# Kernel tuning notes

Hardware: AMD Instinct MI355X
Metric: run time of the kernel (lower is better)

The kernel has to match this reference:

```python
import jax, jax.numpy as jnp
import numpy as np

B, NS, NW, L, DL, DS, OUT, VOCAB = 32, 8, 32, 196, 1024, 2048, 512, 3266
SCALE = 0.05


def setup_inputs() -> dict:
    key = jax.random.key(0)
    ks = jax.random.split(key, 15)
    r = lambda k, shape: jax.random.normal(k, shape, dtype=jnp.float32)
    return {
        "local_features": r(ks[0], (B, DL, L)),
        "sentenc": r(ks[1], (B, NS, DS)),
        "W_s": r(ks[2], (L, DS)) * SCALE,
        "W_v": r(ks[3], (L, DL)) * SCALE,
        "W_a": r(ks[4], (1, L)) * SCALE,
        "W_ih1": r(ks[5], (4 * OUT, DL)) * SCALE,
        "W_hh1": r(ks[6], (4 * OUT, OUT)) * SCALE,
        "b_ih1": r(ks[7], (4 * OUT,)) * SCALE,
        "b_hh1": r(ks[8], (4 * OUT,)) * SCALE,
        "W_ih2": r(ks[9], (4 * OUT, OUT)) * SCALE,
        "W_hh2": r(ks[10], (4 * OUT, OUT)) * SCALE,
        "b_ih2": r(ks[11], (4 * OUT,)) * SCALE,
        "b_hh2": r(ks[12], (4 * OUT,)) * SCALE,
        "W_f": r(ks[13], (VOCAB, OUT)) * SCALE,
        "b_f": r(ks[14], (VOCAB,)) * SCALE,
    }


def _lstm_cell(x, h, c, W_ih, W_hh, b_ih, b_hh):
    # PyTorch LSTMCell: gates order i, f, g, o
    gates = x @ W_ih.T + b_ih + h @ W_hh.T + b_hh
    i, f, g, o = jnp.split(gates, 4, axis=-1)
    c_new = jax.nn.sigmoid(f) * c + jax.nn.sigmoid(i) * jnp.tanh(g)
    h_new = jax.nn.sigmoid(o) * jnp.tanh(c_new)
    return h_new, c_new


def reference(local_features, sentenc, W_s, W_v, W_a,
              W_ih1, W_hh1, b_ih1, b_hh1,
              W_ih2, W_hh2, b_ih2, b_hh2, W_f, b_f):
    # ---- additive (Bahdanau-style) attention, vectorized over sentences ----
    sent = jnp.einsum('bns,ls->bnl', sentenc, W_s)           # [B,NS,L]
    vis = jnp.einsum('bdi,ld->bil', local_features, W_v)     # [B,L(loc i),L(out l)]
    tot = jnp.tanh(vis[:, None, :, :] + sent[:, :, :, None]) # [B,NS,L,L]
    a = jnp.einsum('bnil,l->bni', tot, W_a[0])                # [B,NS,L]
    # original code: softmax over a size-1 trailing dim -> all-ones weights
    a_soft = jax.nn.softmax(a[..., None], axis=-1)[..., 0]    # [B,NS,L], == 1.0
    final = jnp.einsum('bni,bdi->bnd', a_soft, local_features)  # [B,NS,DL]

    # ---- dual-LSTMCell decoder: same attended input repeated NW times ----
    xs = jnp.broadcast_to(final[:, :, None, :], (B, NS, NW, DL))
    xs = xs.reshape(B, NS * NW, DL).transpose(1, 0, 2)        # [T,B,DL]

    def step(carry, x):
        h, c, h1, c1 = carry
        h, c = _lstm_cell(x, h, c, W_ih1, W_hh1, b_ih1, b_hh1)
        h1, c1 = _lstm_cell(h, h1, c1, W_ih2, W_hh2, b_ih2, b_hh2)
        word = h1 @ W_f.T + b_f
        return (h, c, h1, c1), word

    z = jnp.zeros((B, OUT), dtype=local_features.dtype)
    _, words = jax.lax.scan(step, (z, z, z, z), xs)           # [T,B,VOCAB]
    word_list = words.reshape(NS, NW, B, VOCAB).transpose(2, 0, 1, 3)
    return word_list
```

## Files before the change

kernel.cpp:

```cpp
#include <hip/hip_runtime.h>
#include <hip/hip_bf16.h>

#define B_     32
#define DL_    1024
#define L_     196
#define OUT_   512
#define G4_    2048
#define T_     256
#define VOCAB_ 3266
#define NWG_L1  16
#define NWG_L2  64
#define NWG_REC (NWG_L1 + NWG_L2)
#define NSL_    8

#define SIG_STRIDE_ (NSL_ * 16)
#define SIG_Q_      (257 * SIG_STRIDE_ * 4)
#define OFF_SH   0
#define OFF_SH1  (SIG_Q_)
#define OFF_SR2  (OFF_SH1 + 2 * SIG_Q_)
#define OFF_X    (OFF_SR2 + SIG_Q_)
#define OFF_XW1  (OFF_X + B_*DL_*4)
#define OFF_B2   (OFF_XW1 + B_*G4_*4)
#define OFF_HP   (OFF_B2 + G4_*4)
#define OFF_H1   (OFF_HP + 8*B_*OUT_*2)

typedef _Float16 half8 __attribute__((ext_vector_type(8)));
typedef float floatx4 __attribute__((ext_vector_type(4)));

__device__ __forceinline__ float sigmf(float v) { return 1.0f / (1.0f + __expf(-v)); }

__device__ __forceinline__ unsigned short f2h(float f) {
  union { _Float16 h; unsigned short u; } c;
  c.h = (_Float16)f;
  return c.u;
}

__device__ __forceinline__ half8 ldw8(const float* p) {
  float4 q0 = *(const float4*)p;
  float4 q1 = *(const float4*)(p + 4);
  half8 r;
  r[0] = (_Float16)q0.x; r[1] = (_Float16)q0.y; r[2] = (_Float16)q0.z; r[3] = (_Float16)q0.w;
  r[4] = (_Float16)q1.x; r[5] = (_Float16)q1.y; r[6] = (_Float16)q1.z; r[7] = (_Float16)q1.w;
  return r;
}

__device__ __forceinline__ half8 pack8(float4 a, float4 b) {
  half8 r;
  r[0] = (_Float16)a.x; r[1] = (_Float16)a.y; r[2] = (_Float16)a.z; r[3] = (_Float16)a.w;
  r[4] = (_Float16)b.x; r[5] = (_Float16)b.y; r[6] = (_Float16)b.z; r[7] = (_Float16)b.w;
  return r;
}

__device__ __forceinline__ unsigned long long ld8(const unsigned long long* p) {
  return __hip_atomic_load(p, __ATOMIC_RELAXED, __HIP_MEMORY_SCOPE_AGENT);
}
__device__ __forceinline__ void st8(unsigned long long* p, unsigned long long v) {
  __hip_atomic_store(p, v, __ATOMIC_RELAXED, __HIP_MEMORY_SCOPE_AGENT);
}

__device__ __forceinline__ void sigraw(unsigned int* p) {
  __hip_atomic_fetch_add(p, 1u, __ATOMIC_RELAXED, __HIP_MEMORY_SCOPE_AGENT);
}

__device__ __forceinline__ void pollge(unsigned int* p, unsigned tgt, unsigned* dead) {
  if (*dead) return;
  unsigned polls = 0;
  while (__hip_atomic_load(p, __ATOMIC_RELAXED, __HIP_MEMORY_SCOPE_AGENT) < tgt) {
    __builtin_amdgcn_s_sleep(2);
    if (++polls > 400000u) { *dead = 1; break; }
  }
}

__global__ __launch_bounds__(256) void k_rowsum(const float* __restrict__ lf, float* __restrict__ x) {
  int t = blockIdx.x * 256 + threadIdx.x;
  const float4* p = (const float4*)(lf + (size_t)t * L_);
  float s = 0.f;
  #pragma unroll
  for (int i = 0; i < 49; ++i) { float4 v = p[i]; s += (v.x + v.y) + (v.z + v.w); }
  x[t] = s;
}

__global__ __launch_bounds__(256) void k_xw1(const float* __restrict__ x, const float* __restrict__ Wih1,
                                             const float* __restrict__ bih1, const float* __restrict__ bhh1,
                                             const float* __restrict__ bih2, const float* __restrict__ bhh2,
                                             float* __restrict__ xw1, float* __restrict__ bias2) {
  int t = blockIdx.x * 256 + threadIdx.x;
  int b = t >> 11, j = t & (G4_ - 1);
  const float4* xp = (const float4*)(x + (size_t)b * DL_);
  const float4* wp = (const float4*)(Wih1 + (size_t)j * DL_);
  float s = 0.f;
  #pragma unroll 8
  for (int i = 0; i < DL_ / 4; ++i) {
    float4 a = xp[i], w = wp[i];
    s += a.x * w.x + a.y * w.y + a.z * w.z + a.w * w.w;
  }
  xw1[t] = s + bih1[j] + bhh1[j];
  if (t < G4_) bias2[t] = bih2[t] + bhh2[t];
}

__global__ __launch_bounds__(256, 1) void k_rec(const float* __restrict__ Whh1,
                                                const float* __restrict__ Wih2,
                                                const float* __restrict__ Whh2,
                                                const float* __restrict__ xw1,
                                                const float* __restrict__ bias2,
                                                unsigned short* __restrict__ Hp,
                                                unsigned short* __restrict__ H1,
                                                unsigned int* __restrict__ sh,
                                                unsigned int* __restrict__ sh1,
                                                unsigned int* __restrict__ sr2) {
  __shared__ __align__(16) unsigned short sm[17408];
  unsigned long long* smu = (unsigned long long*)sm;
  const int wg = blockIdx.x, tid = threadIdx.x;
  unsigned dead = 0;
  unsigned long long* Hpu = (unsigned long long*)Hp;
  unsigned long long* H1u = (unsigned long long*)H1;
  const int wv = tid >> 6, l = tid & 63, lr = l & 15, kg = l >> 4;
  const int swz = lr & 7;

  if (wg < NWG_L1) {
    const int u0 = (wg * 4 + wv) * 8;
    half8 wfa[16], wfb[16];
    {
      const int ja = (lr & 3) * 512 + u0 + (lr >> 2);
      const int jb = (lr & 3) * 512 + (u0 + 4) + (lr >> 2);
      const float* wra = Whh1 + (size_t)ja * OUT_ + kg * 8;
      const float* wrb = Whh1 + (size_t)jb * OUT_ + kg * 8;
      #pragma unroll
      for (int kt = 0; kt < 16; ++kt) { wfa[kt] = ldw8(wra + kt * 32); wfb[kt] = ldw8(wrb + kt * 32); }
    }
    floatx4 xb00, xb01, xb10, xb11;
    #pragma unroll
    for (int g = 0; g < 4; ++g) {
      xb00[g] = xw1[lr * G4_ + g * OUT_ + u0 + kg];
      xb01[g] = xw1[(16 + lr) * G4_ + g * OUT_ + u0 + kg];
      xb10[g] = xw1[lr * G4_ + g * OUT_ + u0 + 4 + kg];
      xb11[g] = xw1[(16 + lr) * G4_ + g * OUT_ + u0 + 4 + kg];
    }
    float cs00 = 0.f, cs01 = 0.f, cs10 = 0.f, cs11 = 0.f;

    for (int q = 0; q < T_; ++q) {
      if (q > 0) {
        if (tid < 8) pollge(&sh[q * SIG_STRIDE_ + tid * 16], 2, &dead);
        else if (tid >= 16 && tid < 24 && q >= 8)
          pollge(&sr2[(q - 7) * SIG_STRIDE_ + (tid - 16) * 16], 8, &dead);
        __syncthreads();
      }
      const unsigned long long* src = Hpu + (size_t)(q & 7) * 4096;
      unsigned long long v[16];
      #pragma unroll
      for (int i = 0; i < 16; ++i) v[i] = ld8(src + i * 256 + tid);
      #pragma unroll
      for (int i = 0; i < 16; ++i) {
        int w = i * 256 + tid;
        int b = w >> 7, c8 = w & 127, k8 = c8 >> 1, hf = c8 & 1;
        smu[b * 128 + ((k8 ^ (b & 7)) << 1) + hf] = v[i];
      }
      __syncthreads();

      floatx4 a00 = xb00, a01 = xb01, a10 = xb10, a11 = xb11;
      #pragma unroll
      for (int kt = 0; kt < 16; ++kt) {
        int c0 = ((kt * 4 + kg) ^ swz) * 8;
        half8 h0 = *(const half8*)&sm[lr * 512 + c0];
        half8 h1 = *(const half8*)&sm[(16 + lr) * 512 + c0];
        a00 = __builtin_amdgcn_mfma_f32_16x16x32_f16(wfa[kt], h0, a00, 0, 0, 0);
        a01 = __builtin_amdgcn_mfma_f32_16x16x32_f16(wfa[kt], h1, a01, 0, 0, 0);
        a10 = __builtin_amdgcn_mfma_f32_16x16x32_f16(wfb[kt], h0, a10, 0, 0, 0);
        a11 = __builtin_amdgcn_mfma_f32_16x16x32_f16(wfb[kt], h1, a11, 0, 0, 0);
      }
      {
        float i0, f0, g0, o0;
        i0 = sigmf(a00[0]); f0 = sigmf(a00[1]); g0 = tanhf(a00[2]); o0 = sigmf(a00[3]);
        cs00 = fmaf(f0, cs00, i0 * g0);
        sm[16384 + lr * 32 + wv * 8 + kg] = f2h(o0 * tanhf(cs00));
        i0 = sigmf(a01[0]); f0 = sigmf(a01[1]); g0 = tanhf(a01[2]); o0 = sigmf(a01[3]);
        cs01 = fmaf(f0, cs01, i0 * g0);
        sm[16384 + (16 + lr) * 32 + wv * 8 + kg] = f2h(o0 * tanhf(cs01));
        i0 = sigmf(a10[0]); f0 = sigmf(a10[1]); g0 = tanhf(a10[2]); o0 = sigmf(a10[3]);
        cs10 = fmaf(f0, cs10, i0 * g0);
        sm[16384 + lr * 32 + wv * 8 + 4 + kg] = f2h(o0 * tanhf(cs10));
        i0 = sigmf(a11[0]); f0 = sigmf(a11[1]); g0 = tanhf(a11[2]); o0 = sigmf(a11[3]);
        cs11 = fmaf(f0, cs11, i0 * g0);
        sm[16384 + (16 + lr) * 32 + wv * 8 + 4 + kg] = f2h(o0 * tanhf(cs11));
      }
      __syncthreads();
      {
        int row = tid >> 3, chunk = tid & 7;
        st8(Hpu + (size_t)((q + 1) & 7) * 4096 + (size_t)row * 128 + wg * 8 + chunk,
            smu[4096 + row * 8 + chunk]);
      }
      __syncthreads();
      if (tid == 0) sigraw(&sh[(q + 1) * SIG_STRIDE_ + (wg & 7) * 16]);
    }
  } else {
    const int wl = wg - NWG_L1;
    const int half = wl & 1;
    const int ub = wl >> 1;
    const int b0 = half * 16;
    const int u0 = (ub * 4 + wv) * 4;
    const int slot2 = (wl >> 1) & 7;
    half8 wf[32];
    {
      const int j = (lr & 3) * 512 + u0 + (lr >> 2);
      const float* wi = Wih2 + (size_t)j * OUT_ + kg * 8;
      const float* wh = Whh2 + (size_t)j * OUT_ + kg * 8;
      #pragma unroll
      for (int kt = 0; kt < 16; ++kt) wf[kt] = ldw8(wi + kt * 32);
      #pragma unroll
      for (int kt = 0; kt < 16; ++kt) wf[16 + kt] = ldw8(wh + kt * 32);
    }
    floatx4 bs;
    #pragma unroll
    for (int g = 0; g < 4; ++g) bs[g] = bias2[g * OUT_ + u0 + kg];
    float cs = 0.f;

    for (int q = 1; q <= T_; ++q) {
      if (tid < 8) pollge(&sh[q * SIG_STRIDE_ + tid * 16], 2, &dead);
      else if (tid >= 8 && tid < 16 && q >= 2)
        pollge(&sh1[(q - 1) * 2 * SIG_STRIDE_ + half * SIG_STRIDE_ + (tid - 8) * 16], 4, &dead);
      __syncthreads();

      const unsigned long long* shp  = Hpu + (size_t)(q & 7) * 4096;
      const unsigned long long* sh1p = H1u + (size_t)(q - 1) * 4096;
      unsigned long long v[16];
      #pragma unroll
      for (int i = 0; i < 16; ++i) {
        int w = i * 256 + tid;
        int row = w >> 8, c8 = w & 255, k8 = c8 >> 1, hf = c8 & 1;
        v[i] = (k8 < 64) ? ld8(shp  + (size_t)(b0 + row) * 128 + (k8 << 1) + hf)
                         : ld8(sh1p + (size_t)(b0 + row) * 128 + ((k8 - 64) << 1) + hf);
      }
      #pragma unroll
      for (int i = 0; i < 16; ++i) {
        int w = i * 256 + tid;
        int row = w >> 8, c8 = w & 255, k8 = c8 >> 1, hf = c8 & 1;
        smu[row * 256 + ((k8 ^ (row & 7)) << 1) + hf] = v[i];
      }
      __syncthreads();
      if (tid == 0) sigraw(&sr2[q * SIG_STRIDE_ + (wg & 7) * 16]);

      floatx4 a0 = bs;
      #pragma unroll
      for (int kt = 0; kt < 32; ++kt) {
        int c0 = ((kt * 4 + kg) ^ swz) * 8;
        half8 xv = *(const half8*)&sm[lr * 1024 + c0];
        a0 = __builtin_amdgcn_mfma_f32_16x16x32_f16(wf[kt], xv, a0, 0, 0, 0);
      }
      {
        float i0 = sigmf(a0[0]), f0 = sigmf(a0[1]), g0 = tanhf(a0[2]), o0 = sigmf(a0[3]);
        cs = fmaf(f0, cs, i0 * g0);
        float h1v = o0 * tanhf(cs);
        sm[16384 + lr * 16 + wv * 4 + kg] = f2h(h1v);
      }
      __syncthreads();
      if (tid < 64) {
        int row = tid >> 2, uw = tid & 3;
        st8(H1u + (size_t)q * 4096 + (size_t)(b0 + row) * 128 + ub * 4 + uw,
            smu[4096 + row * 4 + uw]);
      }
      __syncthreads();
      if (tid == 0) sigraw(&sh1[q * 2 * SIG_STRIDE_ + half * SIG_STRIDE_ + slot2 * 16]);
    }
  }
}

__global__ __launch_bounds__(256, 2) void k_gemm(const unsigned short* __restrict__ H1,
                                                 const float* __restrict__ Wf,
                                                 const float* __restrict__ bfv,
                                                 float* __restrict__ out) {
  __shared__ __align__(16) unsigned short Asm[128 * 56];
  __shared__ __align__(16) unsigned short Bsm[128 * 56];
  const int mt = blockIdx.x, nt = blockIdx.y, tid = threadIdx.x;
  const int wv = tid >> 6, l = tid & 63, lr = l & 15, kg = l >> 4;
  floatx4 acc[2][8];
  #pragma unroll
  for (int m = 0; m < 2; ++m)
    #pragma unroll
    for (int n = 0; n < 8; ++n) acc[m][n] = (floatx4){0.f, 0.f, 0.f, 0.f};

  const unsigned short* Abase = H1 + (size_t)(32 + mt * 128) * OUT_;
  const int r = tid >> 1, kh = (tid & 1) * 16;
  const int vr = nt * 128 + r;

  for (int k0 = 0; k0 < OUT_; k0 += 32) {
    {
      const uint4* srcA = (const uint4*)(Abase + (size_t)r * OUT_ + k0 + kh);
      uint4 a0 = srcA[0], a1 = srcA[1];
      *(uint4*)&Asm[r * 56 + kh]     = a0;
      *(uint4*)&Asm[r * 56 + kh + 8] = a1;
    }
    {
      float4 f0 = {0,0,0,0}, f1 = f0, f2 = f0, f3 = f0;
      if (vr < VOCAB_) {
        const float4* wsrc = (const float4*)(Wf + (size_t)vr * OUT_ + k0 + kh);
        f0 = wsrc[0]; f1 = wsrc[1]; f2 = wsrc[2]; f3 = wsrc[3];
      }
      *(half8*)&Bsm[r * 56 + kh]     = pack8(f0, f1);
      *(half8*)&Bsm[r * 56 + kh + 8] = pack8(f2, f3);
    }
    __syncthreads();

    const int co = kg * 8;
    half8 a0f = *(const half8*)&Asm[(wv * 32 + lr) * 56 + co];
    half8 a1f = *(const half8*)&Asm[(wv * 32 + 16 + lr) * 56 + co];
    #pragma unroll
    for (int n = 0; n < 8; ++n) {
      half8 bf = *(const half8*)&Bsm[(n * 16 + lr) * 56 + co];
      acc[0][n] = __builtin_amdgcn_mfma_f32_16x16x32_f16(a0f, bf, acc[0][n], 0, 0, 0);
      acc[1][n] = __builtin_amdgcn_mfma_f32_16x16x32_f16(a1f, bf, acc[1][n], 0, 0, 0);
    }
    __syncthreads();
  }

  #pragma unroll
  for (int n = 0; n < 8; ++n) {
    int vcol = nt * 128 + n * 16 + lr;
    if (vcol >= VOCAB_) continue;
    float bias = bfv[vcol];
    #pragma unroll
    for (int m = 0; m < 2; ++m)
      #pragma unroll
      for (int g = 0; g < 4; ++g) {
        int mg = mt * 128 + wv * 32 + m * 16 + kg * 4 + g;
        int bb = mg & 31, s = mg >> 5;
        out[(size_t)(bb * 256 + s) * VOCAB_ + vcol] = acc[m][n][g] + bias;
      }
  }
}

extern "C" void kernel_launch(void* const* d_in, const int* in_sizes, int n_in,
                              void* d_out, int out_size, void* d_ws, size_t ws_size,
                              hipStream_t stream) {
  const float* lf   = (const float*)d_in[0];
  const float* Wih1 = (const float*)d_in[5];
  const float* Whh1 = (const float*)d_in[6];
  const float* bih1 = (const float*)d_in[7];
  const float* bhh1 = (const float*)d_in[8];
  const float* Wih2 = (const float*)d_in[9];
  const float* Whh2 = (const float*)d_in[10];
  const float* bih2 = (const float*)d_in[11];
  const float* bhh2 = (const float*)d_in[12];
  const float* Wf   = (const float*)d_in[13];
  const float* bfv  = (const float*)d_in[14];
  float* out = (float*)d_out;
  char* ws = (char*)d_ws;

  unsigned int*   sh   = (unsigned int*)(ws + OFF_SH);
  unsigned int*   sh1  = (unsigned int*)(ws + OFF_SH1);
  unsigned int*   sr2  = (unsigned int*)(ws + OFF_SR2);
  float*          x    = (float*)(ws + OFF_X);
  float*          xw1  = (float*)(ws + OFF_XW1);
  float*          b2   = (float*)(ws + OFF_B2);
  unsigned short* Hp   = (unsigned short*)(ws + OFF_HP);
  unsigned short* H1   = (unsigned short*)(ws + OFF_H1);

  (void)hipMemsetAsync(ws, 0, OFF_X, stream);
  (void)hipMemsetAsync(Hp, 0, 8 * B_ * OUT_ * 2, stream);
  (void)hipMemsetAsync(H1, 0, B_ * OUT_ * 2, stream);

  k_rowsum<<<128, 256, 0, stream>>>(lf, x);
  k_xw1<<<256, 256, 0, stream>>>(x, Wih1, bih1, bhh1, bih2, bhh2, xw1, b2);

  void* kargs[] = {(void*)&Whh1, (void*)&Wih2, (void*)&Whh2, (void*)&xw1, (void*)&b2,
                   (void*)&Hp, (void*)&H1, (void*)&sh, (void*)&sh1, (void*)&sr2};
  hipError_t cerr = hipLaunchCooperativeKernel((void*)k_rec, dim3(NWG_REC), dim3(256),
                                               kargs, 0, stream);
  if (cerr != hipSuccess) {
    k_rec<<<NWG_REC, 256, 0, stream>>>(Whh1, Wih2, Whh2, xw1, b2, Hp, H1, sh, sh1, sr2);
  }

  k_gemm<<<dim3(64, 26), 256, 0, stream>>>(H1, Wf, bfv, out);
}
```

Before: 1.164 ms.

## Split layer-2 input staging by dependency and narrow publish barriers to one wave

Layer-2 workgroups now wait only for the previous step's layer-2 hidden state, load and stage it into shared memory, and only then wait for the current layer-1 hidden state before loading it. This overlaps the H1 load with the wait for the layer-1 signal. Both layers also restrict the global store of their new hidden state to the first wave, which issues an s_waitcnt before signalling. That removes one block-wide barrier per step from the critical path. The risk is memory-ordering correctness, because the waitcnt inside one wave stands in for a full barrier before the flag is raised.

```diff
diff --git a/kernel.cpp b/kernel.cpp
--- a/kernel.cpp
+++ b/kernel.cpp
@@ -184,13 +184,17 @@
         sm[16384 + (16 + lr) * 32 + wv * 8 + 4 + kg] = f2h(o0 * tanhf(cs11));
       }
       __syncthreads();
-      {
-        int row = tid >> 3, chunk = tid & 7;
-        st8(Hpu + (size_t)((q + 1) & 7) * 4096 + (size_t)row * 128 + wg * 8 + chunk,
-            smu[4096 + row * 8 + chunk]);
-      }
-      __syncthreads();
-      if (tid == 0) sigraw(&sh[(q + 1) * SIG_STRIDE_ + (wg & 7) * 16]);
+      if (tid < 64) {
+        #pragma unroll
+        for (int j = 0; j < 4; ++j) {
+          int idx = j * 64 + tid;
+          int row = idx >> 3, chunk = idx & 7;
+          st8(Hpu + (size_t)((q + 1) & 7) * 4096 + (size_t)row * 128 + wg * 8 + chunk,
+              smu[4096 + row * 8 + chunk]);
+        }
+        asm volatile("s_waitcnt vmcnt(0)" ::: "memory");
+        if (tid == 0) sigraw(&sh[(q + 1) * SIG_STRIDE_ + (wg & 7) * 16]);
+      }
     }
   } else {
     const int wl = wg - NWG_L1;
@@ -215,26 +219,43 @@
     float cs = 0.f;
 
     for (int q = 1; q <= T_; ++q) {
-      if (tid < 8) pollge(&sh[q * SIG_STRIDE_ + tid * 16], 2, &dead);
-      else if (tid >= 8 && tid < 16 && q >= 2)
-        pollge(&sh1[(q - 1) * 2 * SIG_STRIDE_ + half * SIG_STRIDE_ + (tid - 8) * 16], 4, &dead);
-      __syncthreads();
-
       const unsigned long long* shp  = Hpu + (size_t)(q & 7) * 4096;
       const unsigned long long* sh1p = H1u + (size_t)(q - 1) * 4096;
-      unsigned long long v[16];
-      #pragma unroll
-      for (int i = 0; i < 16; ++i) {
-        int w = i * 256 + tid;
-        int row = w >> 8, c8 = w & 255, k8 = c8 >> 1, hf = c8 & 1;
-        v[i] = (k8 < 64) ? ld8(shp  + (size_t)(b0 + row) * 128 + (k8 << 1) + hf)
-                         : ld8(sh1p + (size_t)(b0 + row) * 128 + ((k8 - 64) << 1) + hf);
-      }
-      #pragma unroll
-      for (int i = 0; i < 16; ++i) {
-        int w = i * 256 + tid;
-        int row = w >> 8, c8 = w & 255, k8 = c8 >> 1, hf = c8 & 1;
-        smu[row * 256 + ((k8 ^ (row & 7)) << 1) + hf] = v[i];
+
+      if (tid >= 8 && tid < 16 && q >= 2)
+        pollge(&sh1[(q - 1) * 2 * SIG_STRIDE_ + half * SIG_STRIDE_ + (tid - 8) * 16], 4, &dead);
+      __syncthreads();
+
+      unsigned long long v1[8];
+      #pragma unroll
+      for (int i = 0; i < 8; ++i) {
+        int w = i * 256 + tid;
+        int row = w >> 7, c8 = w & 127;
+        v1[i] = ld8(sh1p + (size_t)(b0 + row) * 128 + c8);
+      }
+      #pragma unroll
+      for (int i = 0; i < 8; ++i) {
+        int w = i * 256 + tid;
+        int row = w >> 7, c8 = w & 127;
+        int k8 = 64 + (c8 >> 1), hf = c8 & 1;
+        smu[row * 256 + ((k8 ^ (row & 7)) << 1) + hf] = v1[i];
+      }
+      if (tid < 8) pollge(&sh[q * SIG_STRIDE_ + tid * 16], 2, &dead);
+      __syncthreads();
+
+      unsigned long long v0[8];
+      #pragma unroll
+      for (int i = 0; i < 8; ++i) {
+        int w = i * 256 + tid;
+        int row = w >> 7, c8 = w & 127;
+        v0[i] = ld8(shp + (size_t)(b0 + row) * 128 + c8);
+      }
+      #pragma unroll
+      for (int i = 0; i < 8; ++i) {
+        int w = i * 256 + tid;
+        int row = w >> 7, c8 = w & 127;
+        int k8 = c8 >> 1, hf = c8 & 1;
+        smu[row * 256 + ((k8 ^ (row & 7)) << 1) + hf] = v0[i];
       }
       __syncthreads();
       if (tid == 0) sigraw(&sr2[q * SIG_STRIDE_ + (wg & 7) * 16]);
@@ -257,9 +278,9 @@
         int row = tid >> 2, uw = tid & 3;
         st8(H1u + (size_t)q * 4096 + (size_t)(b0 + row) * 128 + ub * 4 + uw,
             smu[4096 + row * 4 + uw]);
-      }
-      __syncthreads();
-      if (tid == 0) sigraw(&sh1[q * 2 * SIG_STRIDE_ + half * SIG_STRIDE_ + slot2 * 16]);
+        asm volatile("s_waitcnt vmcnt(0)" ::: "memory");
+        if (tid == 0) sigraw(&sh1[q * 2 * SIG_STRIDE_ + half * SIG_STRIDE_ + slot2 * 16]);
+      }
     }
   }
 }
```

Result: slower. 1.195 ms (+2.7%).
